# Performance work log

Hardware: AMD Instinct MI355X
Metric: run time of the kernel (lower is better)

## Reference

```python
import jax, jax.numpy as jnp
import numpy as np

N_NODES = 50000
N_EDGES = 600000
D_IN = 128
D_HID = 128
D_OUT = 64


def _graph_conv(x, src, dst, W, b, n):
    """DGL GraphConv, norm='both': out = D_in^{-1/2} A D_out^{-1/2} x W + b,
    degrees clamped to min 1. Weight applied before aggregation (equivalent,
    and what DGL does when in_feats >= out_feats)."""
    ones = jnp.ones(src.shape[0], x.dtype)
    deg_out = jnp.clip(jax.ops.segment_sum(ones, src, num_segments=n), 1.0)
    deg_in = jnp.clip(jax.ops.segment_sum(ones, dst, num_segments=n), 1.0)
    h = (x * jax.lax.rsqrt(deg_out)[:, None]) @ W          # [n, d_out]
    agg = jax.ops.segment_sum(h[src], dst, num_segments=n)  # SpMM: gather + scatter-add
    return agg * jax.lax.rsqrt(deg_in)[:, None] + b


def setup_inputs() -> dict:
    key = jax.random.key(0)
    ks = jax.random.split(key, 9)
    features = jax.random.normal(ks[0], (N_NODES, D_IN), jnp.float32)
    src1 = jax.random.randint(ks[1], (N_EDGES,), 0, N_NODES, jnp.int32)
    dst1 = jax.random.randint(ks[2], (N_EDGES,), 0, N_NODES, jnp.int32)
    src2 = jax.random.randint(ks[3], (N_EDGES,), 0, N_NODES, jnp.int32)
    dst2 = jax.random.randint(ks[4], (N_EDGES,), 0, N_NODES, jnp.int32)
    order_attn = jax.random.uniform(ks[5], (2,), jnp.float32)
    W1 = jax.random.normal(ks[6], (D_IN, D_HID), jnp.float32) * 0.05
    b1 = jnp.zeros((D_HID,), jnp.float32)
    W2 = jax.random.normal(ks[7], (D_HID, D_OUT), jnp.float32) * 0.05
    b2 = jnp.zeros((D_OUT,), jnp.float32)
    return {"features": features, "src1": src1, "dst1": dst1,
            "src2": src2, "dst2": dst2, "order_attn": order_attn,
            "W1": W1, "b1": b1, "W2": W2, "b2": b2}


def reference(features, src1, dst1, src2, dst2, order_attn, W1, b1, W2, b2):
    n = features.shape[0]
    # layer 1 on both graphs + weighted order-attention combine
    x11 = _graph_conv(features, src1, dst1, W1, b1, n)
    x12 = _graph_conv(features, src2, dst2, W1, b1, n)
    x1 = order_attn[0] * x11 + order_attn[1] * x12
    # layer 2 on both graphs + weighted combine
    x21 = _graph_conv(x1, src1, dst1, W2, b2, n)
    x22 = _graph_conv(x1, src2, dst2, W2, b2, n)
    return order_attn[0] * x21 + order_attn[1] * x22
```

## Files before the change

### kernel.cpp

```cpp
#include <hip/hip_runtime.h>

#define DINF 128
#define DHID 128
#define DOUTF 64

#define CHUNK 12544
#define NCHUNK 4
#define ECH 16

typedef unsigned short ushort_t;
typedef unsigned int uint_t;
typedef __attribute__((ext_vector_type(8))) short bf16x8;
typedef __attribute__((ext_vector_type(4))) float f32x4;

__device__ __forceinline__ ushort_t f2b(float x) {
    uint_t u = __float_as_uint(x);
    u += 0x7fffu + ((u >> 16) & 1u);
    return (ushort_t)(u >> 16);
}
__device__ __forceinline__ float b2f_lo(uint_t u) { return __uint_as_float(u << 16); }
__device__ __forceinline__ float b2f_hi(uint_t u) { return __uint_as_float(u & 0xffff0000u); }

__global__ void deg_priv_kernel(const int* __restrict__ s1, const int* __restrict__ d1,
                                const int* __restrict__ s2, const int* __restrict__ d2,
                                int* __restrict__ deg, int N, int ne) {
    extern __shared__ int h[];
    int t = threadIdx.x;
    for (int j = t; j < CHUNK; j += 1024) h[j] = 0;
    __syncthreads();

    const int* p = blockIdx.z == 0 ? s1 : blockIdx.z == 1 ? d1 : blockIdx.z == 2 ? s2 : d2;
    int lo = blockIdx.y * CHUNK;
    int per = (ne + ECH - 1) / ECH;
    int e0 = blockIdx.x * per;
    int e1 = e0 + per < ne ? e0 + per : ne;
    for (int i = e0 + t; i < e1; i += 1024) {
        int idx = p[i] - lo;
        if ((unsigned)idx < (unsigned)CHUNK) atomicAdd(&h[idx], 1);
    }
    __syncthreads();

    int* dz = deg + (size_t)blockIdx.z * N;
    for (int j = t; j < CHUNK; j += 1024) {
        int node = lo + j;
        int v = h[j];
        if (v && node < N) atomicAdd(&dz[node], v);
    }
}

__global__ void scan1_kernel(const int* __restrict__ d1i, const int* __restrict__ d2i,
                             int* __restrict__ offs, int* __restrict__ bsum, int n) {
    __shared__ int warp_sums[4];
    int t = threadIdx.x;
    int lane = t & 63;
    int wid = t >> 6;
    int base = blockIdx.x * 1024 + t * 4;

    int v[4];
    int tot = 0;
    #pragma unroll
    for (int j = 0; j < 4; ++j) {
        int i = base + j;
        int d = (i < n) ? d1i[i] + d2i[i] : 0;
        v[j] = d; tot += d;
    }
    int x = tot;
    #pragma unroll
    for (int off = 1; off < 64; off <<= 1) {
        int y = __shfl_up(x, off, 64);
        if (lane >= off) x += y;
    }
    if (lane == 63) warp_sums[wid] = x;
    __syncthreads();
    int wbase = 0;
    for (int w = 0; w < wid; ++w) wbase += warp_sums[w];
    int run = wbase + x - tot;
    #pragma unroll
    for (int j = 0; j < 4; ++j) {
        int i = base + j;
        if (i < n) offs[i] = run;
        run += v[j];
    }
    if (t == 255) bsum[blockIdx.x] = run;
}

__global__ void scan2_kernel(int* __restrict__ bsum, int* __restrict__ offs, int nb, int n) {
    int lane = threadIdx.x;
    int run = 0;
    for (int base = 0; base < nb; base += 64) {
        int i = base + lane;
        int v = (i < nb) ? bsum[i] : 0;
        int x = v;
        #pragma unroll
        for (int off = 1; off < 64; off <<= 1) {
            int y = __shfl_up(x, off, 64);
            if (lane >= off) x += y;
        }
        if (i < nb) bsum[i] = run + x - v;
        run += __shfl(x, 63, 64);
    }
    if (lane == 0) offs[n] = run;
}

__global__ void scan3_kernel(int* __restrict__ offs, int* __restrict__ cursor,
                             const int* __restrict__ bsum, int n) {
    int base = blockIdx.x * 1024 + threadIdx.x * 4;
    int add = bsum[blockIdx.x];
    #pragma unroll
    for (int j = 0; j < 4; ++j) {
        int i = base + j;
        if (i < n) { int o = offs[i] + add; offs[i] = o; cursor[i] = o; }
    }
}

__global__ void fill_kernel(const int* __restrict__ src, const int* __restrict__ dst,
                            const int* __restrict__ deg_out, const int* __restrict__ deg_in,
                            const float* __restrict__ attn, int ai,
                            int* __restrict__ cursor, int2* __restrict__ csr, int ne) {
    int i = blockIdx.x * 256 + threadIdx.x;
    if (i >= ne) return;
    int s = src[i];
    int d = dst[i];
    int pos = atomicAdd(&cursor[d], 1);
    float w = attn[ai] * rsqrtf(fmaxf((float)deg_in[d], 1.0f))
                       * rsqrtf(fmaxf((float)deg_out[s], 1.0f));
    csr[pos] = make_int2(s, __float_as_int(w));
}

__global__ void wconv_kernel(const float* __restrict__ W, ushort_t* __restrict__ Wt,
                             int K, int Nc) {
    int tid = blockIdx.x * 256 + threadIdx.x;
    if (tid >= K * Nc) return;
    int ncol = tid / K, k = tid % K;
    Wt[tid] = f2b(W[(size_t)k * Nc + ncol]);
}

template<int NOUT, bool F32IN>
__global__ __launch_bounds__(256) void mfma_gemm_kernel(const void* __restrict__ Xv,
                                                        const ushort_t* __restrict__ Wt,
                                                        ushort_t* __restrict__ Y, int n) {
    constexpr int CT = NOUT / 16;
    const int lane = threadIdx.x & 63;
    const int wv = threadIdx.x >> 6;
    const int row0 = blockIdx.x * 64 + wv * 16;
    const int arow = row0 + (lane & 15);
    const int arc = arow < n ? arow : (n - 1);

    f32x4 acc[CT];
    #pragma unroll
    for (int ct = 0; ct < CT; ++ct) acc[ct] = (f32x4)(0.f);

    #pragma unroll
    for (int kk = 0; kk < 4; ++kk) {
        const int k0 = kk * 32 + (lane >> 4) * 8;
        bf16x8 a;
        if (F32IN) {
            const float* xp = (const float*)Xv + (size_t)arc * 128 + k0;
            float4 u0 = *(const float4*)xp;
            float4 u1 = *(const float4*)(xp + 4);
            a[0] = (short)f2b(u0.x); a[1] = (short)f2b(u0.y);
            a[2] = (short)f2b(u0.z); a[3] = (short)f2b(u0.w);
            a[4] = (short)f2b(u1.x); a[5] = (short)f2b(u1.y);
            a[6] = (short)f2b(u1.z); a[7] = (short)f2b(u1.w);
        } else {
            a = *(const bf16x8*)((const ushort_t*)Xv + (size_t)arc * 128 + k0);
        }
        #pragma unroll
        for (int ct = 0; ct < CT; ++ct) {
            bf16x8 b = *(const bf16x8*)(Wt + (size_t)(ct * 16 + (lane & 15)) * 128 + k0);
            acc[ct] = __builtin_amdgcn_mfma_f32_16x16x32_bf16(a, b, acc[ct], 0, 0, 0);
        }
    }

    const int orow0 = row0 + (lane >> 4) * 4;
    const int col = lane & 15;
    #pragma unroll
    for (int ct = 0; ct < CT; ++ct) {
        #pragma unroll
        for (int r = 0; r < 4; ++r) {
            int row = orow0 + r;
            if (row < n) Y[(size_t)row * NOUT + ct * 16 + col] = f2b(acc[ct][r]);
        }
    }
}

__global__ void agg128_kernel(const ushort_t* __restrict__ V, const int* __restrict__ offs,
                              const int2* __restrict__ csr, const float* __restrict__ bias,
                              const float* __restrict__ attn, uint_t* __restrict__ out, int n) {
    int wid = (int)(((size_t)blockIdx.x * blockDim.x + threadIdx.x) >> 6);
    int lane = threadIdx.x & 63;
    if (wid >= n) return;
    int e0 = offs[wid], e1 = offs[wid + 1];

    float acc0 = 0.f, acc1 = 0.f;

    int e = e0;
    for (; e + 4 <= e1; e += 4) {
        int2 c0v = csr[e + 0], c1v = csr[e + 1], c2v = csr[e + 2], c3v = csr[e + 3];
        float w0 = __int_as_float(c0v.y), w1 = __int_as_float(c1v.y);
        float w2 = __int_as_float(c2v.y), w3 = __int_as_float(c3v.y);
        uint_t u0 = ((const uint_t*)(V + (size_t)c0v.x * 128))[lane];
        uint_t u1 = ((const uint_t*)(V + (size_t)c1v.x * 128))[lane];
        uint_t u2 = ((const uint_t*)(V + (size_t)c2v.x * 128))[lane];
        uint_t u3 = ((const uint_t*)(V + (size_t)c3v.x * 128))[lane];
        acc0 += w0 * b2f_lo(u0); acc1 += w0 * b2f_hi(u0);
        acc0 += w1 * b2f_lo(u1); acc1 += w1 * b2f_hi(u1);
        acc0 += w2 * b2f_lo(u2); acc1 += w2 * b2f_hi(u2);
        acc0 += w3 * b2f_lo(u3); acc1 += w3 * b2f_hi(u3);
    }
    for (; e < e1; ++e) {
        int2 cv = csr[e];
        float w = __int_as_float(cv.y);
        uint_t u = ((const uint_t*)(V + (size_t)cv.x * 128))[lane];
        acc0 += w * b2f_lo(u); acc1 += w * b2f_hi(u);
    }

    float bs = attn[0] + attn[1];
    float2 bb = ((const float2*)bias)[lane];
    float o0 = acc0 + bs * bb.x;
    float o1 = acc1 + bs * bb.y;
    out[(size_t)wid * 64 + lane] = (uint_t)f2b(o0) | ((uint_t)f2b(o1) << 16);
}

__global__ void agg64_kernel(const ushort_t* __restrict__ V, const int* __restrict__ offs,
                             const int2* __restrict__ csr, const float* __restrict__ bias,
                             const float* __restrict__ attn, float* __restrict__ out, int n) {
    int wid = (int)(((size_t)blockIdx.x * blockDim.x + threadIdx.x) >> 6);
    int lane = threadIdx.x & 63;
    if (wid >= n) return;
    int e0 = offs[wid], e1 = offs[wid + 1];

    float acc = 0.f;

    int e = e0;
    for (; e + 4 <= e1; e += 4) {
        int2 c0v = csr[e + 0], c1v = csr[e + 1], c2v = csr[e + 2], c3v = csr[e + 3];
        float w0 = __int_as_float(c0v.y), w1 = __int_as_float(c1v.y);
        float w2 = __int_as_float(c2v.y), w3 = __int_as_float(c3v.y);
        float g0 = __uint_as_float(((uint_t)V[(size_t)c0v.x * 64 + lane]) << 16);
        float g1 = __uint_as_float(((uint_t)V[(size_t)c1v.x * 64 + lane]) << 16);
        float g2 = __uint_as_float(((uint_t)V[(size_t)c2v.x * 64 + lane]) << 16);
        float g3 = __uint_as_float(((uint_t)V[(size_t)c3v.x * 64 + lane]) << 16);
        acc += w0 * g0 + w1 * g1 + w2 * g2 + w3 * g3;
    }
    for (; e < e1; ++e) {
        int2 cv = csr[e];
        float w = __int_as_float(cv.y);
        float g = __uint_as_float(((uint_t)V[(size_t)cv.x * 64 + lane]) << 16);
        acc += w * g;
    }

    float bs = attn[0] + attn[1];
    out[(size_t)wid * 64 + lane] = acc + bs * bias[lane];
}

extern "C" void kernel_launch(void* const* d_in, const int* in_sizes, int n_in,
                              void* d_out, int out_size, void* d_ws, size_t ws_size,
                              hipStream_t stream) {
    const float* feat = (const float*)d_in[0];
    const int* src1   = (const int*)d_in[1];
    const int* dst1   = (const int*)d_in[2];
    const int* src2   = (const int*)d_in[3];
    const int* dst2   = (const int*)d_in[4];
    const float* attn = (const float*)d_in[5];
    const float* W1   = (const float*)d_in[6];
    const float* b1   = (const float*)d_in[7];
    const float* W2   = (const float*)d_in[8];
    const float* b2   = (const float*)d_in[9];
    float* out = (float*)d_out;

    const int N  = in_sizes[0] / DINF;
    const int NE = in_sizes[1];
    const int NB = (N + 1023) / 1024;

    ushort_t* Wt1 = (ushort_t*)d_ws;
    ushort_t* Wt2 = Wt1 + 128 * 128;
    ushort_t* A   = Wt2 + 64 * 128;
    ushort_t* B   = A + (size_t)N * DHID;
    ushort_t* C   = B + (size_t)N * DHID;
    int2* csr   = (int2*)(C + (size_t)N * DOUTF);
    int* offs   = (int*)(csr + 2 * (size_t)NE);
    int* cursor = offs + (N + 1);
    int* deg    = cursor + N;
    int* d1o = deg;
    int* d1i = deg + N;
    int* d2o = deg + 2 * (size_t)N;
    int* d2i = deg + 3 * (size_t)N;
    int* bsum = deg + 4 * (size_t)N;

    hipMemsetAsync(deg, 0, sizeof(int) * 4 * (size_t)N, stream);

    wconv_kernel<<<(128 * 128 + 255) / 256, 256, 0, stream>>>(W1, Wt1, 128, 128);
    wconv_kernel<<<(128 * 64 + 255) / 256, 256, 0, stream>>>(W2, Wt2, 128, 64);

    deg_priv_kernel<<<dim3(ECH, NCHUNK, 4), 1024, CHUNK * sizeof(int), stream>>>(
        src1, dst1, src2, dst2, deg, N, NE);

    scan1_kernel<<<NB, 256, 0, stream>>>(d1i, d2i, offs, bsum, N);
    scan2_kernel<<<1, 64, 0, stream>>>(bsum, offs, NB, N);
    scan3_kernel<<<NB, 256, 0, stream>>>(offs, cursor, bsum, N);

    int eb = (NE + 255) / 256;
    fill_kernel<<<eb, 256, 0, stream>>>(src1, dst1, d1o, d1i, attn, 0, cursor, csr, NE);
    fill_kernel<<<eb, 256, 0, stream>>>(src2, dst2, d2o, d2i, attn, 1, cursor, csr, NE);

    int gb = (N + 63) / 64;
    mfma_gemm_kernel<DHID, true><<<gb, 256, 0, stream>>>(feat, Wt1, A, N);
    agg128_kernel<<<(N + 3) / 4, 256, 0, stream>>>(A, offs, csr, b1, attn, (uint_t*)B, N);

    mfma_gemm_kernel<DOUTF, false><<<gb, 256, 0, stream>>>(B, Wt2, C, N);
    agg64_kernel<<<(N + 3) / 4, 256, 0, stream>>>(C, offs, csr, b2, attn, out, N);
}
```

Baseline: 234.8 us.

## Merge weight-convert and CSR-fill launches, deepen gather batching in aggregation kernels

The two weight-conversion launches become one kernel, and the two per-graph CSR fill launches become a single 2D-grid launch, which removes launch gaps. The 128-wide aggregation now batches 8 edges per iteration so more independent gathers are in flight. The 64-wide aggregation splits the wave into two halves that each process alternate edges with 4-byte loads, then combines the halves with a cross-lane shuffle. This doubles useful bytes per lane load but adds a reduction and idles half the lanes during the store.

```diff
diff --git a/kernel.cpp b/kernel.cpp
--- a/kernel.cpp
+++ b/kernel.cpp
@@ -113,26 +113,36 @@
     }
 }
 
-__global__ void fill_kernel(const int* __restrict__ src, const int* __restrict__ dst,
-                            const int* __restrict__ deg_out, const int* __restrict__ deg_in,
-                            const float* __restrict__ attn, int ai,
-                            int* __restrict__ cursor, int2* __restrict__ csr, int ne) {
+__global__ void fill2_kernel(const int* __restrict__ src1, const int* __restrict__ dst1,
+                             const int* __restrict__ src2, const int* __restrict__ dst2,
+                             const int* __restrict__ deg, const float* __restrict__ attn,
+                             int* __restrict__ cursor, int2* __restrict__ csr, int N, int ne) {
     int i = blockIdx.x * 256 + threadIdx.x;
     if (i >= ne) return;
+    int g = blockIdx.y;
+    const int* src = g == 0 ? src1 : src2;
+    const int* dst = g == 0 ? dst1 : dst2;
+    const int* deg_out = deg + (size_t)(2 * g) * N;
+    const int* deg_in  = deg + (size_t)(2 * g + 1) * N;
     int s = src[i];
     int d = dst[i];
     int pos = atomicAdd(&cursor[d], 1);
-    float w = attn[ai] * rsqrtf(fmaxf((float)deg_in[d], 1.0f))
-                       * rsqrtf(fmaxf((float)deg_out[s], 1.0f));
+    float w = attn[g] * rsqrtf(fmaxf((float)deg_in[d], 1.0f))
+                      * rsqrtf(fmaxf((float)deg_out[s], 1.0f));
     csr[pos] = make_int2(s, __float_as_int(w));
 }
 
-__global__ void wconv_kernel(const float* __restrict__ W, ushort_t* __restrict__ Wt,
-                             int K, int Nc) {
+__global__ void wconv2_kernel(const float* __restrict__ W1, const float* __restrict__ W2,
+                              ushort_t* __restrict__ Wt1, ushort_t* __restrict__ Wt2) {
     int tid = blockIdx.x * 256 + threadIdx.x;
-    if (tid >= K * Nc) return;
-    int ncol = tid / K, k = tid % K;
-    Wt[tid] = f2b(W[(size_t)k * Nc + ncol]);
+    if (tid < 128 * 128) {
+        int ncol = tid / 128, k = tid % 128;
+        Wt1[tid] = f2b(W1[(size_t)k * 128 + ncol]);
+    } else if (tid < 128 * 128 + 64 * 128) {
+        int t2 = tid - 128 * 128;
+        int ncol = t2 / 128, k = t2 % 128;
+        Wt2[t2] = f2b(W2[(size_t)k * 64 + ncol]);
+    }
 }
 
 template<int NOUT, bool F32IN>
@@ -195,18 +205,36 @@
     float acc0 = 0.f, acc1 = 0.f;
 
     int e = e0;
-    for (; e + 4 <= e1; e += 4) {
-        int2 c0v = csr[e + 0], c1v = csr[e + 1], c2v = csr[e + 2], c3v = csr[e + 3];
-        float w0 = __int_as_float(c0v.y), w1 = __int_as_float(c1v.y);
-        float w2 = __int_as_float(c2v.y), w3 = __int_as_float(c3v.y);
-        uint_t u0 = ((const uint_t*)(V + (size_t)c0v.x * 128))[lane];
-        uint_t u1 = ((const uint_t*)(V + (size_t)c1v.x * 128))[lane];
-        uint_t u2 = ((const uint_t*)(V + (size_t)c2v.x * 128))[lane];
-        uint_t u3 = ((const uint_t*)(V + (size_t)c3v.x * 128))[lane];
-        acc0 += w0 * b2f_lo(u0); acc1 += w0 * b2f_hi(u0);
-        acc0 += w1 * b2f_lo(u1); acc1 += w1 * b2f_hi(u1);
-        acc0 += w2 * b2f_lo(u2); acc1 += w2 * b2f_hi(u2);
-        acc0 += w3 * b2f_lo(u3); acc1 += w3 * b2f_hi(u3);
+    for (; e + 8 <= e1; e += 8) {
+        int2 cv[8];
+        uint_t u[8];
+        #pragma unroll
+        for (int j = 0; j < 8; ++j) cv[j] = csr[e + j];
+        #pragma unroll
+        for (int j = 0; j < 8; ++j)
+            u[j] = ((const uint_t*)(V + (size_t)cv[j].x * 128))[lane];
+        #pragma unroll
+        for (int j = 0; j < 8; ++j) {
+            float w = __int_as_float(cv[j].y);
+            acc0 += w * b2f_lo(u[j]);
+            acc1 += w * b2f_hi(u[j]);
+        }
+    }
+    if (e + 4 <= e1) {
+        int2 cv[4];
+        uint_t u[4];
+        #pragma unroll
+        for (int j = 0; j < 4; ++j) cv[j] = csr[e + j];
+        #pragma unroll
+        for (int j = 0; j < 4; ++j)
+            u[j] = ((const uint_t*)(V + (size_t)cv[j].x * 128))[lane];
+        #pragma unroll
+        for (int j = 0; j < 4; ++j) {
+            float w = __int_as_float(cv[j].y);
+            acc0 += w * b2f_lo(u[j]);
+            acc1 += w * b2f_hi(u[j]);
+        }
+        e += 4;
     }
     for (; e < e1; ++e) {
         int2 cv = csr[e];
@@ -227,31 +255,51 @@
                              const float* __restrict__ attn, float* __restrict__ out, int n) {
     int wid = (int)(((size_t)blockIdx.x * blockDim.x + threadIdx.x) >> 6);
     int lane = threadIdx.x & 63;
+    int half = lane >> 5;
+    int hl = lane & 31;
     if (wid >= n) return;
     int e0 = offs[wid], e1 = offs[wid + 1];
 
-    float acc = 0.f;
+    float acc0 = 0.f, acc1 = 0.f;
 
     int e = e0;
-    for (; e + 4 <= e1; e += 4) {
-        int2 c0v = csr[e + 0], c1v = csr[e + 1], c2v = csr[e + 2], c3v = csr[e + 3];
-        float w0 = __int_as_float(c0v.y), w1 = __int_as_float(c1v.y);
-        float w2 = __int_as_float(c2v.y), w3 = __int_as_float(c3v.y);
-        float g0 = __uint_as_float(((uint_t)V[(size_t)c0v.x * 64 + lane]) << 16);
-        float g1 = __uint_as_float(((uint_t)V[(size_t)c1v.x * 64 + lane]) << 16);
-        float g2 = __uint_as_float(((uint_t)V[(size_t)c2v.x * 64 + lane]) << 16);
-        float g3 = __uint_as_float(((uint_t)V[(size_t)c3v.x * 64 + lane]) << 16);
-        acc += w0 * g0 + w1 * g1 + w2 * g2 + w3 * g3;
-    }
-    for (; e < e1; ++e) {
+    for (; e + 8 <= e1; e += 8) {
+        int2 cv[4];
+        uint_t u[4];
+        #pragma unroll
+        for (int j = 0; j < 4; ++j) cv[j] = csr[e + 2 * j + half];
+        #pragma unroll
+        for (int j = 0; j < 4; ++j)
+            u[j] = ((const uint_t*)(V + (size_t)cv[j].x * 64))[hl];
+        #pragma unroll
+        for (int j = 0; j < 4; ++j) {
+            float w = __int_as_float(cv[j].y);
+            acc0 += w * b2f_lo(u[j]);
+            acc1 += w * b2f_hi(u[j]);
+        }
+    }
+    for (; e + 2 <= e1; e += 2) {
+        int2 cv = csr[e + half];
+        float w = __int_as_float(cv.y);
+        uint_t u = ((const uint_t*)(V + (size_t)cv.x * 64))[hl];
+        acc0 += w * b2f_lo(u); acc1 += w * b2f_hi(u);
+    }
+    if (e < e1 && half == 0) {
         int2 cv = csr[e];
         float w = __int_as_float(cv.y);
-        float g = __uint_as_float(((uint_t)V[(size_t)cv.x * 64 + lane]) << 16);
-        acc += w * g;
-    }
-
-    float bs = attn[0] + attn[1];
-    out[(size_t)wid * 64 + lane] = acc + bs * bias[lane];
+        uint_t u = ((const uint_t*)(V + (size_t)cv.x * 64))[hl];
+        acc0 += w * b2f_lo(u); acc1 += w * b2f_hi(u);
+    }
+
+    acc0 += __shfl_xor(acc0, 32, 64);
+    acc1 += __shfl_xor(acc1, 32, 64);
+
+    if (half == 0) {
+        float bs = attn[0] + attn[1];
+        float2 bb = ((const float2*)bias)[hl];
+        float2 o = make_float2(acc0 + bs * bb.x, acc1 + bs * bb.y);
+        ((float2*)(out + (size_t)wid * 64))[hl] = o;
+    }
 }
 
 extern "C" void kernel_launch(void* const* d_in, const int* in_sizes, int n_in,
@@ -282,16 +330,13 @@
     int* offs   = (int*)(csr + 2 * (size_t)NE);
     int* cursor = offs + (N + 1);
     int* deg    = cursor + N;
-    int* d1o = deg;
     int* d1i = deg + N;
-    int* d2o = deg + 2 * (size_t)N;
     int* d2i = deg + 3 * (size_t)N;
     int* bsum = deg + 4 * (size_t)N;
 
     hipMemsetAsync(deg, 0, sizeof(int) * 4 * (size_t)N, stream);
 
-    wconv_kernel<<<(128 * 128 + 255) / 256, 256, 0, stream>>>(W1, Wt1, 128, 128);
-    wconv_kernel<<<(128 * 64 + 255) / 256, 256, 0, stream>>>(W2, Wt2, 128, 64);
+    wconv2_kernel<<<(128 * 128 + 64 * 128 + 255) / 256, 256, 0, stream>>>(W1, W2, Wt1, Wt2);
 
     deg_priv_kernel<<<dim3(ECH, NCHUNK, 4), 1024, CHUNK * sizeof(int), stream>>>(
         src1, dst1, src2, dst2, deg, N, NE);
@@ -301,8 +346,8 @@
     scan3_kernel<<<NB, 256, 0, stream>>>(offs, cursor, bsum, N);
 
     int eb = (NE + 255) / 256;
-    fill_kernel<<<eb, 256, 0, stream>>>(src1, dst1, d1o, d1i, attn, 0, cursor, csr, NE);
-    fill_kernel<<<eb, 256, 0, stream>>>(src2, dst2, d2o, d2i, attn, 1, cursor, csr, NE);
+    fill2_kernel<<<dim3(eb, 2), 256, 0, stream>>>(src1, dst1, src2, dst2, deg, attn,
+                                                  cursor, csr, N, NE);
 
     int gb = (N + 63) / 64;
     mfma_gemm_kernel<DHID, true><<<gb, 256, 0, stream>>>(feat, Wt1, A, N);
```

New measurement: 212.9 us. -9.3%, faster.
